# Kernel tuning notes

Measured on AMD Instinct MI355X. Metric: run time of the kernel, lower is better.

The kernel has to match this reference:

```python
import jax, jax.numpy as jnp
import numpy as np

EPS_BN = 1e-5      # torch BatchNorm2d default eps
EPS_NORM = 1e-12   # torch F.normalize default eps
NEG_FILL = -1e18


def _bn(h, gamma, beta, mean, var):
    # eval-mode BatchNorm2d over channel axis 1 of NCHW
    scale = (gamma / jnp.sqrt(var + EPS_BN))[None, :, None, None]
    return h * scale + (beta - mean * gamma / jnp.sqrt(var + EPS_BN))[None, :, None, None]


def _l2norm(v, axis):
    n = jnp.linalg.norm(v, axis=axis, keepdims=True)
    return v / jnp.maximum(n, EPS_NORM)


def setup_inputs() -> dict:
    key = jax.random.key(0)
    ks = jax.random.split(key, 6)
    bs, num, dim, K = 16, 8192, 128, 64
    return {
        "x_": jax.random.normal(ks[0], (bs, num, dim), jnp.float32),
        "conv1_w": jax.random.normal(ks[1], (dim, 1, 3, 3), jnp.float32) * 0.1,
        "bn1_gamma": jnp.ones((dim,), jnp.float32),
        "bn1_beta": jnp.zeros((dim,), jnp.float32),
        "bn1_mean": jnp.zeros((dim,), jnp.float32),
        "bn1_var": jnp.ones((dim,), jnp.float32),
        "conv2_w": jax.random.normal(ks[2], (K, dim, 1, 1), jnp.float32) * 0.05,
        "conv2_b": jax.random.normal(ks[3], (K,), jnp.float32) * 0.05,
        "bn2_gamma": jnp.ones((K,), jnp.float32),
        "bn2_beta": jnp.zeros((K,), jnp.float32),
        "bn2_mean": jnp.zeros((K,), jnp.float32),
        "bn2_var": jnp.ones((K,), jnp.float32),
        "centroids": 0.1 * jax.random.uniform(ks[4], (K, dim), jnp.float32),
        "length": jax.random.randint(ks[5], (bs,), 1, num + 1).astype(jnp.int32),
    }


def reference(x_, conv1_w, bn1_gamma, bn1_beta, bn1_mean, bn1_var,
              conv2_w, conv2_b, bn2_gamma, bn2_beta, bn2_mean, bn2_var,
              centroids, length):
    N, T, C = x_.shape
    K = centroids.shape[0]
    # [N, T, C] -> [N, C, T, 1] (input_modal='textual'/'region' branch)
    x = jnp.transpose(x_, (0, 2, 1))[..., None]
    # descriptor-wise L2 norm over channels (normalize_input=True)
    x = _l2norm(x, axis=1)
    # depthwise 3x3 conv, padding 1, no bias
    h = jax.lax.conv_general_dilated(
        x, conv1_w, window_strides=(1, 1), padding=((1, 1), (1, 1)),
        dimension_numbers=("NCHW", "OIHW", "NCHW"), feature_group_count=C)
    h = jax.nn.relu(_bn(h, bn1_gamma, bn1_beta, bn1_mean, bn1_var))
    # pointwise 1x1 conv (as matmul) + bias
    h = jnp.einsum("ncto,kc->nkto", h, conv2_w[:, :, 0, 0]) + conv2_b[None, :, None, None]
    h = jax.nn.relu(_bn(h, bn2_gamma, bn2_beta, bn2_mean, bn2_var))
    soft_assign = h.reshape(N, K, T)
    # textual path: mask padded positions before softmax over clusters
    valid = jnp.arange(T)[None, :] < length[:, None]          # [N, T]
    soft_assign = jnp.where(valid[:, None, :], soft_assign, NEG_FILL)
    a = jax.nn.softmax(soft_assign, axis=1)                   # [N, K, T]
    x_flat = x[..., 0]                                        # [N, C, T]
    # fused VLAD: sum_t a[n,k,t]*(x[n,c,t] - centroid[k,c]) as two matmuls
    vlad = jnp.einsum("nkt,nct->nkc", a, x_flat) - a.sum(-1)[:, :, None] * centroids[None]
    vlad = _l2norm(vlad, axis=2)           # intra-normalization
    vlad = vlad.reshape(N, K * x_flat.shape[1])
    vlad = _l2norm(vlad, axis=1)           # global L2 norm
    return vlad
```

## Files before the change

kernel.cpp:

```cpp
#include <hip/hip_runtime.h>
#include <math.h>

#define N_ 16
#define T_ 8192
#define C_ 128
#define K_ 64

#define TPB_A 128
#define BPN_A 64

#define NW_ASUM 0
#define NW_GSUM 1024
#define NW_MCS  2048
#define NW_W2F  4096
#define NW_P1   8192
#define NW_XTM  8960
#define NW_PART 8397568
#define NW_TOTAL 16786176

typedef __attribute__((ext_vector_type(8))) short short8;
typedef __attribute__((ext_vector_type(4))) float f32x4;

__device__ __forceinline__ uint bfr(float f) {
    uint u = __float_as_uint(f);
    return (u + 0x7fffu + ((u >> 16) & 1u)) >> 16;
}
__device__ __forceinline__ uint pack2(float lo, float hi) {
    return bfr(lo) | (bfr(hi) << 16);
}
__device__ __forceinline__ float bfu(ushort u) {
    return __uint_as_float(((uint)u) << 16);
}

__global__ void setup_k(const float* __restrict__ conv1_w,
                        const float* __restrict__ bn1_g, const float* __restrict__ bn1_b,
                        const float* __restrict__ bn1_m, const float* __restrict__ bn1_v,
                        const float* __restrict__ conv2_w,
                        const float* __restrict__ bn2_g, const float* __restrict__ bn2_v,
                        ushort* __restrict__ w2t, float* __restrict__ p1,
                        float* __restrict__ zr, int zcnt) {
    const int gt = blockIdx.x * 256 + threadIdx.x;
    for (int idx = gt; idx < 8192; idx += 1024) {
        int j = idx & 7;
        int lane = (idx >> 3) & 63;
        int mq = idx >> 9;
        int m = mq >> 2, q = mq & 3;
        int fr = lane & 15, fg = lane >> 4;
        int k = m * 16 + fr;
        float sck = bn2_g[k] * rsqrtf(bn2_v[k] + 1e-5f);
        float v = conv2_w[k * C_ + q * 32 + fg * 8 + j] * sck;
        w2t[idx] = (ushort)bfr(v);
    }
    for (int c = gt; c < C_; c += 1024) {
        float s1 = bn1_g[c] * rsqrtf(bn1_v[c] + 1e-5f);
        p1[c]       = conv1_w[c * 9 + 1] * s1;
        p1[128 + c] = conv1_w[c * 9 + 4] * s1;
        p1[256 + c] = conv1_w[c * 9 + 7] * s1;
        p1[384 + c] = bn1_b[c] - bn1_m[c] * s1;
    }
    for (int i = gt; i < zcnt; i += 1024) zr[i] = 0.0f;
}

__global__ __launch_bounds__(256, 8) void xnorm_k(const float* __restrict__ x,
                                                  ushort* __restrict__ xtm,
                                                  const int* __restrict__ length,
                                                  float* __restrict__ mcs) {
    __shared__ uint xt[32][64];
    const int tid = threadIdx.x;
    const int lane = tid & 63;
    const int w = tid >> 6;
    const int n = blockIdx.x >> 8;
    const int tloc = (blockIdx.x & 255) * 32;
    const size_t row0 = (size_t)blockIdx.x * 32;
    const int L = length[n];
    const int Lb = ((L + 127) >> 7) << 7;

#pragma unroll
    for (int i = 0; i < 8; ++i) {
        int r = w * 8 + i;
        const float* xr = x + (row0 + r) * C_;
        float2 v = *(const float2*)&xr[lane * 2];
        float ss = v.x * v.x + v.y * v.y;
#pragma unroll
        for (int m = 1; m < 64; m <<= 1) ss += __shfl_xor(ss, m, 64);
        float rn = 1.0f / fmaxf(sqrtf(ss), 1e-12f);
        xt[r][lane] = pack2(v.x * rn, v.y * rn);
    }
    __syncthreads();

    if (tloc <= Lb) {
        uint4* dst = (uint4*)(xtm + (size_t)blockIdx.x * 4096);
#pragma unroll
        for (int uu = 0; uu < 2; ++uu) {
            int u = tid * 2 + uu;
            int c = u >> 2, j = u & 3;
            int cw = c >> 1, sh = (c & 1) * 16;
            uint o[4];
#pragma unroll
            for (int q = 0; q < 4; ++q) {
                uint lo = (xt[j * 8 + q * 2][cw] >> sh) & 0xffffu;
                uint hi = (xt[j * 8 + q * 2 + 1][cw] >> sh) & 0xffffu;
                o[q] = lo | (hi << 16);
            }
            uint4 v; v.x = o[0]; v.y = o[1]; v.z = o[2]; v.w = o[3];
            dst[u] = v;
        }
    }
    if (tloc >= Lb && w == 0) {
        float sx = 0.f, sy = 0.f;
#pragma unroll 8
        for (int r = 0; r < 32; ++r) {
            uint u = xt[r][lane];
            sx += bfu((ushort)(u & 0xffffu));
            sy += bfu((ushort)(u >> 16));
        }
        atomicAdd(&mcs[n * C_ + lane * 2], sx);
        atomicAdd(&mcs[n * C_ + lane * 2 + 1], sy);
    }
}

__global__ __launch_bounds__(256, 3) void fused_k(
    const ushort* __restrict__ xtm,
    const float* __restrict__ conv2_b,
    const float* __restrict__ bn2_g, const float* __restrict__ bn2_b,
    const float* __restrict__ bn2_m, const float* __restrict__ bn2_v,
    const int* __restrict__ length,
    const ushort* __restrict__ w2t, const float* __restrict__ p1,
    float* __restrict__ part, float* __restrict__ asum) {

    __shared__ __align__(16) ushort w2l[8192];
    __shared__ __align__(16) ushort h_s[4][16 * 136];
    __shared__ __align__(16) uint4 ab[2][64 * 5];

    const int tid = threadIdx.x;
    const int lane = tid & 63;
    const int w = tid >> 6;
    const int fr = lane & 15, fg = lane >> 4;
    const int tile = w >> 1, half = w & 1;
    const int n = blockIdx.x >> 6;
    const int blk = blockIdx.x & (BPN_A - 1);
    const int tb = blk * TPB_A;
    const int L = length[n];
    if (tb >= L) return;

    const ushort* xtm_n = xtm + (size_t)n * 256 * 4096;

    {
        const uint4* w2g = (const uint4*)w2t;
        uint4* w2d = (uint4*)w2l;
#pragma unroll
        for (int i = 0; i < 4; ++i) w2d[tid + i * 256] = w2g[tid + i * 256];
    }

    float wa[2], wbv[2], wcv[2], sbv[2];
#pragma unroll
    for (int p = 0; p < 2; ++p) {
        int c = lane + p * 64;
        wa[p] = p1[c]; wbv[p] = p1[128 + c];
        wcv[p] = p1[256 + c]; sbv[p] = p1[384 + c];
    }

    float sh2r[16];
#pragma unroll
    for (int m = 0; m < 4; ++m)
#pragma unroll
        for (int r = 0; r < 4; ++r) {
            int k = m * 16 + fg * 4 + r;
            float s = bn2_g[k] * rsqrtf(bn2_v[k] + 1e-5f);
            sh2r[m * 4 + r] = s * conv2_b[k] + bn2_b[k] - bn2_m[k] * s;
        }

    short8 onesf;
    {
        short f = (fr == 0) ? (short)0x3F80 : (short)0;
#pragma unroll
        for (int j = 0; j < 8; ++j) onesf[j] = f;
    }

    f32x4 accB[9];
#pragma unroll
    for (int cb = 0; cb < 9; ++cb) accB[cb] = (f32x4){0.f, 0.f, 0.f, 0.f};

    __syncthreads();

    for (int s = 0; s < TPB_A / 64; ++s) {
        const int tbs = tb + s * 64;
        const int tcs = (tbs >> 5) + tile;
        const ushort* xch = xtm_n + (size_t)tcs * 4096;
        const int t0 = tbs + tile * 32 + half * 16;

        if (t0 < L) {
            ushort* hw = h_s[w];
#pragma unroll
            for (int p = 0; p < 2; ++p) {
                const int c = lane + p * 64;
                short8 x0 = *(const short8*)&xch[c * 32 + half * 16];
                short8 x1 = *(const short8*)&xch[c * 32 + half * 16 + 8];
                float av[18];
                av[0] = 0.f; av[17] = 0.f;
                if (t0 > 0)
                    av[0] = bfu(half ? xch[c * 32 + 15] : xch[c * 32 - 4096 + 31]);
                if (t0 + 16 < T_)
                    av[17] = bfu(half ? xch[c * 32 + 4096] : xch[c * 32 + 16]);
#pragma unroll
                for (int j = 0; j < 8; ++j) {
                    av[1 + j] = bfu((ushort)x0[j]);
                    av[9 + j] = bfu((ushort)x1[j]);
                }
                float WA = wa[p], WB = wbv[p], WC = wcv[p], SB = sbv[p];
#pragma unroll
                for (int j = 0; j < 16; ++j)
                    hw[j * 136 + c] = (ushort)bfr(
                        fmaxf(0.f, av[j] * WA + av[j + 1] * WB + av[j + 2] * WC + SB));
            }
            f32x4 accL[4];
#pragma unroll
            for (int m = 0; m < 4; ++m) accL[m] = (f32x4){0.f, 0.f, 0.f, 0.f};
            const ushort* hbp = h_s[w] + fr * 136 + fg * 8;
#pragma unroll
            for (int q = 0; q < 4; ++q) {
                short8 hf = *(const short8*)(hbp + q * 32);
                short8 w0 = *(const short8*)&w2l[((0 * 4 + q) * 64 + lane) * 8];
                short8 w1 = *(const short8*)&w2l[((1 * 4 + q) * 64 + lane) * 8];
                short8 w2f = *(const short8*)&w2l[((2 * 4 + q) * 64 + lane) * 8];
                short8 w3 = *(const short8*)&w2l[((3 * 4 + q) * 64 + lane) * 8];
                accL[0] = __builtin_amdgcn_mfma_f32_16x16x32_bf16(w0, hf, accL[0], 0, 0, 0);
                accL[1] = __builtin_amdgcn_mfma_f32_16x16x32_bf16(w1, hf, accL[1], 0, 0, 0);
                accL[2] = __builtin_amdgcn_mfma_f32_16x16x32_bf16(w2f, hf, accL[2], 0, 0, 0);
                accL[3] = __builtin_amdgcn_mfma_f32_16x16x32_bf16(w3, hf, accL[3], 0, 0, 0);
            }
            {
                int t = t0 + fr;
                float v[16];
#pragma unroll
                for (int m = 0; m < 4; ++m)
#pragma unroll
                    for (int r = 0; r < 4; ++r)
                        v[m * 4 + r] = fmaxf(0.f, accL[m][r] + sh2r[m * 4 + r]);
                if (t < L) {
                    float mx = v[0];
#pragma unroll
                    for (int i = 1; i < 16; ++i) mx = fmaxf(mx, v[i]);
                    mx = fmaxf(mx, __shfl_xor(mx, 16, 64));
                    mx = fmaxf(mx, __shfl_xor(mx, 32, 64));
                    float se = 0.f;
#pragma unroll
                    for (int i = 0; i < 16; ++i) { v[i] = __expf(v[i] - mx); se += v[i]; }
                    se += __shfl_xor(se, 16, 64);
                    se += __shfl_xor(se, 32, 64);
                    float inv = 1.0f / se;
#pragma unroll
                    for (int i = 0; i < 16; ++i) v[i] *= inv;
                } else {
#pragma unroll
                    for (int i = 0; i < 16; ++i) v[i] = 0.015625f;
                }
                const int jq = half * 2 + (fr >> 3);
                const int te = fr & 7;
#pragma unroll
                for (int m = 0; m < 4; ++m)
#pragma unroll
                    for (int r = 0; r < 4; ++r) {
                        int k = m * 16 + fg * 4 + r;
                        ((ushort*)&ab[tile][k * 5 + jq])[te] = (ushort)bfr(v[m * 4 + r]);
                    }
            }
        } else {
            uint4 cfill;
            cfill.x = cfill.y = cfill.z = cfill.w = 0x3C803C80u;
            ab[tile][lane * 5 + half * 2] = cfill;
            ab[tile][lane * 5 + half * 2 + 1] = cfill;
        }
        __syncthreads();
#pragma unroll
        for (int cc = 0; cc < 2; ++cc) {
            const ushort* xc2 = xtm_n + (size_t)((tbs >> 5) + cc) * 4096;
            short8 af = *(const short8*)&ab[cc][(w * 16 + fr) * 5 + fg];
#pragma unroll
            for (int cb = 0; cb < 8; ++cb) {
                short8 bfv = *(const short8*)&xc2[(cb * 16 + fr) * 32 + fg * 8];
                accB[cb] = __builtin_amdgcn_mfma_f32_16x16x32_bf16(af, bfv, accB[cb], 0, 0, 0);
            }
            accB[8] = __builtin_amdgcn_mfma_f32_16x16x32_bf16(af, onesf, accB[8], 0, 0, 0);
        }
        __syncthreads();
    }

    float* pr = part + (size_t)(n * BPN_A + blk) * (K_ * C_);
#pragma unroll
    for (int cb = 0; cb < 8; ++cb)
#pragma unroll
        for (int r = 0; r < 4; ++r)
            pr[(w * 16 + fg * 4 + r) * C_ + cb * 16 + fr] = accB[cb][r];
    if (fr == 0) {
#pragma unroll
        for (int r = 0; r < 4; ++r)
            atomicAdd(&asum[n * K_ + w * 16 + fg * 4 + r], accB[8][r]);
    }
}

__global__ void finalize2_k(const float* __restrict__ cent,
                            const float* __restrict__ part,
                            const float* __restrict__ asum,
                            const float* __restrict__ mcs,
                            const int* __restrict__ length,
                            float* __restrict__ gsum, float* __restrict__ out) {
    int row = blockIdx.x * 4 + (threadIdx.x >> 6);
    int lane = threadIdx.x & 63;
    int n = row >> 6, k = row & 63;
    const int L = length[n];
    const int nlive = (L + 127) >> 7;
    const float* pr = part + (size_t)n * BPN_A * (K_ * C_) + k * C_;
    float y0 = 0.f, y1 = 0.f;
#pragma unroll 4
    for (int b = 0; b < nlive; ++b) {
        y0 += pr[(size_t)b * (K_ * C_) + lane];
        y1 += pr[(size_t)b * (K_ * C_) + lane + 64];
    }
    y0 += 0.015625f * mcs[n * C_ + lane];
    y1 += 0.015625f * mcs[n * C_ + lane + 64];
    float as = asum[row] + (float)(T_ - nlive * 128) * 0.015625f;
    y0 -= as * cent[k * C_ + lane];
    y1 -= as * cent[k * C_ + lane + 64];
    float ss = y0 * y0 + y1 * y1;
#pragma unroll
    for (int m = 1; m < 64; m <<= 1) ss += __shfl_xor(ss, m, 64);
    float rs = 1.0f / fmaxf(sqrtf(ss), 1e-12f);
    out[(size_t)row * C_ + lane] = y0 * rs;
    out[(size_t)row * C_ + lane + 64] = y1 * rs;
    if (lane == 0) atomicAdd(&gsum[n], ss * rs * rs);
}

__global__ void gscale2_k(float* __restrict__ out, const float* __restrict__ gsum) {
    int idx = blockIdx.x * 256 + threadIdx.x;
    int n = idx >> 13;
    out[idx] *= 1.0f / fmaxf(sqrtf(gsum[n]), 1e-12f);
}

extern "C" void kernel_launch(void* const* d_in, const int* in_sizes, int n_in,
                              void* d_out, int out_size, void* d_ws, size_t ws_size,
                              hipStream_t stream) {
    const float* x       = (const float*)d_in[0];
    const float* conv1_w = (const float*)d_in[1];
    const float* bn1_g   = (const float*)d_in[2];
    const float* bn1_b   = (const float*)d_in[3];
    const float* bn1_m   = (const float*)d_in[4];
    const float* bn1_v   = (const float*)d_in[5];
    const float* conv2_w = (const float*)d_in[6];
    const float* conv2_b = (const float*)d_in[7];
    const float* bn2_g   = (const float*)d_in[8];
    const float* bn2_b   = (const float*)d_in[9];
    const float* bn2_m   = (const float*)d_in[10];
    const float* bn2_v   = (const float*)d_in[11];
    const float* cent    = (const float*)d_in[12];
    const int*   length  = (const int*)d_in[13];
    float* out = (float*)d_out;
    float* ws  = (float*)d_ws;

    setup_k<<<4, 256, 0, stream>>>(conv1_w, bn1_g, bn1_b, bn1_m, bn1_v,
                                   conv2_w, bn2_g, bn2_v,
                                   (ushort*)(ws + NW_W2F), ws + NW_P1,
                                   ws, 4096);
    xnorm_k<<<N_ * T_ / 32, 256, 0, stream>>>(x, (ushort*)(ws + NW_XTM),
                                              length, ws + NW_MCS);
    fused_k<<<N_ * BPN_A, 256, 0, stream>>>(
        (const ushort*)(ws + NW_XTM), conv2_b, bn2_g, bn2_b, bn2_m, bn2_v,
        length, (const ushort*)(ws + NW_W2F), ws + NW_P1,
        ws + NW_PART, ws + NW_ASUM);
    finalize2_k<<<(N_ * K_) / 4, 256, 0, stream>>>(
        cent, ws + NW_PART, ws + NW_ASUM, ws + NW_MCS, length,
        ws + NW_GSUM, out);
    gscale2_k<<<(N_ * K_ * C_) / 256, 256, 0, stream>>>(out, ws + NW_GSUM);
}
```

Baseline: 80.85 us.

## Drop global-norm pass via constant scale and fold setup into xnorm kernel

After intra-normalization each of the 64 cluster rows has unit L2 norm, so the global L2 norm is always 8. The final-normalize kernel can therefore apply a constant 0.125 factor directly, which removes the gsum atomics and the separate gscale pass over the output. The weight/BN-parameter setup work moves into the first four blocks of the xnorm kernel, and workspace zeroing becomes a hipMemsetAsync, cutting kernel launches. The constant-scale shortcut assumes no cluster row has near-zero norm, where the eps clamp would make the true global norm differ from 8.

```diff
diff --git a/kernel.cpp b/kernel.cpp
--- a/kernel.cpp
+++ b/kernel.cpp
@@ -10,8 +10,8 @@
 #define BPN_A 64
 
 #define NW_ASUM 0
-#define NW_GSUM 1024
 #define NW_MCS  2048
+#define NW_ZBYTES (4096 * 4)
 #define NW_W2F  4096
 #define NW_P1   8192
 #define NW_XTM  8960
@@ -32,39 +32,15 @@
     return __uint_as_float(((uint)u) << 16);
 }
 
-__global__ void setup_k(const float* __restrict__ conv1_w,
-                        const float* __restrict__ bn1_g, const float* __restrict__ bn1_b,
-                        const float* __restrict__ bn1_m, const float* __restrict__ bn1_v,
-                        const float* __restrict__ conv2_w,
-                        const float* __restrict__ bn2_g, const float* __restrict__ bn2_v,
-                        ushort* __restrict__ w2t, float* __restrict__ p1,
-                        float* __restrict__ zr, int zcnt) {
-    const int gt = blockIdx.x * 256 + threadIdx.x;
-    for (int idx = gt; idx < 8192; idx += 1024) {
-        int j = idx & 7;
-        int lane = (idx >> 3) & 63;
-        int mq = idx >> 9;
-        int m = mq >> 2, q = mq & 3;
-        int fr = lane & 15, fg = lane >> 4;
-        int k = m * 16 + fr;
-        float sck = bn2_g[k] * rsqrtf(bn2_v[k] + 1e-5f);
-        float v = conv2_w[k * C_ + q * 32 + fg * 8 + j] * sck;
-        w2t[idx] = (ushort)bfr(v);
-    }
-    for (int c = gt; c < C_; c += 1024) {
-        float s1 = bn1_g[c] * rsqrtf(bn1_v[c] + 1e-5f);
-        p1[c]       = conv1_w[c * 9 + 1] * s1;
-        p1[128 + c] = conv1_w[c * 9 + 4] * s1;
-        p1[256 + c] = conv1_w[c * 9 + 7] * s1;
-        p1[384 + c] = bn1_b[c] - bn1_m[c] * s1;
-    }
-    for (int i = gt; i < zcnt; i += 1024) zr[i] = 0.0f;
-}
-
-__global__ __launch_bounds__(256, 8) void xnorm_k(const float* __restrict__ x,
-                                                  ushort* __restrict__ xtm,
-                                                  const int* __restrict__ length,
-                                                  float* __restrict__ mcs) {
+__global__ __launch_bounds__(256, 8) void xnorm_k(
+    const float* __restrict__ x, ushort* __restrict__ xtm,
+    const int* __restrict__ length, float* __restrict__ mcs,
+    const float* __restrict__ conv1_w,
+    const float* __restrict__ bn1_g, const float* __restrict__ bn1_b,
+    const float* __restrict__ bn1_m, const float* __restrict__ bn1_v,
+    const float* __restrict__ conv2_w,
+    const float* __restrict__ bn2_g, const float* __restrict__ bn2_v,
+    ushort* __restrict__ w2t, float* __restrict__ p1) {
     __shared__ uint xt[32][64];
     const int tid = threadIdx.x;
     const int lane = tid & 63;
@@ -74,6 +50,28 @@
     const size_t row0 = (size_t)blockIdx.x * 32;
     const int L = length[n];
     const int Lb = ((L + 127) >> 7) << 7;
+
+    if (blockIdx.x < 4) {
+        const int gt = blockIdx.x * 256 + tid;
+        for (int idx = gt; idx < 8192; idx += 1024) {
+            int j = idx & 7;
+            int ln = (idx >> 3) & 63;
+            int mq = idx >> 9;
+            int m = mq >> 2, q = mq & 3;
+            int fr = ln & 15, fg = ln >> 4;
+            int k = m * 16 + fr;
+            float sck = bn2_g[k] * rsqrtf(bn2_v[k] + 1e-5f);
+            float v = conv2_w[k * C_ + q * 32 + fg * 8 + j] * sck;
+            w2t[idx] = (ushort)bfr(v);
+        }
+        for (int c = gt; c < C_; c += 1024) {
+            float s1 = bn1_g[c] * rsqrtf(bn1_v[c] + 1e-5f);
+            p1[c]       = conv1_w[c * 9 + 1] * s1;
+            p1[128 + c] = conv1_w[c * 9 + 4] * s1;
+            p1[256 + c] = conv1_w[c * 9 + 7] * s1;
+            p1[384 + c] = bn1_b[c] - bn1_m[c] * s1;
+        }
+    }
 
 #pragma unroll
     for (int i = 0; i < 8; ++i) {
@@ -304,7 +302,7 @@
                             const float* __restrict__ asum,
                             const float* __restrict__ mcs,
                             const int* __restrict__ length,
-                            float* __restrict__ gsum, float* __restrict__ out) {
+                            float* __restrict__ out) {
     int row = blockIdx.x * 4 + (threadIdx.x >> 6);
     int lane = threadIdx.x & 63;
     int n = row >> 6, k = row & 63;
@@ -325,16 +323,9 @@
     float ss = y0 * y0 + y1 * y1;
 #pragma unroll
     for (int m = 1; m < 64; m <<= 1) ss += __shfl_xor(ss, m, 64);
-    float rs = 1.0f / fmaxf(sqrtf(ss), 1e-12f);
+    float rs = 0.125f / fmaxf(sqrtf(ss), 1e-12f);
     out[(size_t)row * C_ + lane] = y0 * rs;
     out[(size_t)row * C_ + lane + 64] = y1 * rs;
-    if (lane == 0) atomicAdd(&gsum[n], ss * rs * rs);
-}
-
-__global__ void gscale2_k(float* __restrict__ out, const float* __restrict__ gsum) {
-    int idx = blockIdx.x * 256 + threadIdx.x;
-    int n = idx >> 13;
-    out[idx] *= 1.0f / fmaxf(sqrtf(gsum[n]), 1e-12f);
 }
 
 extern "C" void kernel_launch(void* const* d_in, const int* in_sizes, int n_in,
@@ -357,18 +348,15 @@
     float* out = (float*)d_out;
     float* ws  = (float*)d_ws;
 
-    setup_k<<<4, 256, 0, stream>>>(conv1_w, bn1_g, bn1_b, bn1_m, bn1_v,
-                                   conv2_w, bn2_g, bn2_v,
-                                   (ushort*)(ws + NW_W2F), ws + NW_P1,
-                                   ws, 4096);
-    xnorm_k<<<N_ * T_ / 32, 256, 0, stream>>>(x, (ushort*)(ws + NW_XTM),
-                                              length, ws + NW_MCS);
+    hipMemsetAsync(ws, 0, NW_ZBYTES, stream);
+    xnorm_k<<<N_ * T_ / 32, 256, 0, stream>>>(
+        x, (ushort*)(ws + NW_XTM), length, ws + NW_MCS,
+        conv1_w, bn1_g, bn1_b, bn1_m, bn1_v, conv2_w, bn2_g, bn2_v,
+        (ushort*)(ws + NW_W2F), ws + NW_P1);
     fused_k<<<N_ * BPN_A, 256, 0, stream>>>(
         (const ushort*)(ws + NW_XTM), conv2_b, bn2_g, bn2_b, bn2_m, bn2_v,
         length, (const ushort*)(ws + NW_W2F), ws + NW_P1,
         ws + NW_PART, ws + NW_ASUM);
     finalize2_k<<<(N_ * K_) / 4, 256, 0, stream>>>(
-        cent, ws + NW_PART, ws + NW_ASUM, ws + NW_MCS, length,
-        ws + NW_GSUM, out);
-    gscale2_k<<<(N_ * K_ * C_) / 256, 256, 0, stream>>>(out, ws + NW_GSUM);
-}
+        cent, ws + NW_PART, ws + NW_ASUM, ws + NW_MCS, length, out);
+}
```

After: 71.96 us. 1.12x faster.
